# Kernel optimization log

Measured on AMD Instinct MI355X. Metric: run time of the kernel, lower is better.

## Reference

```python
import jax, jax.numpy as jnp
import numpy as np

B, N_P, N_S, D, H = 8, 512, 512, 512, 8
HD = D // H
SCALE = HD ** -0.5


def setup_inputs() -> dict:
    key = jax.random.key(0)
    ks = jax.random.split(key, 16)
    init = lambda k, shape, fan_in: jax.random.normal(k, shape, jnp.float32) * (1.0 / np.sqrt(fan_in))
    return {
        "piece_embeds": jax.random.normal(ks[0], (B, N_P, D), jnp.float32),
        "slot_embeds": jax.random.normal(ks[1], (B, N_S, D), jnp.float32),
        "mask": jax.random.randint(ks[2], (B, N_P, N_S), 0, 2, jnp.int32),
        "spatial_bias": jax.random.normal(ks[3], (B, N_P, N_S), jnp.float32),
        "Wq": init(ks[4], (D, D), D), "bq": jnp.zeros((D,), jnp.float32),
        "Wk": init(ks[5], (D, D), D), "bk": jnp.zeros((D,), jnp.float32),
        "Wv": init(ks[6], (D, D), D), "bv": jnp.zeros((D,), jnp.float32),
        "Wo": init(ks[7], (D, D), D), "bo": jnp.zeros((D,), jnp.float32),
        "Wc": init(ks[8], (2 * D,), 2 * D), "bc": jnp.zeros((), jnp.float32),
        "Wval": init(ks[9], (D,), D), "bval": jnp.zeros((), jnp.float32),
    }


def reference(piece_embeds, slot_embeds, mask, spatial_bias,
              Wq, bq, Wk, bk, Wv, bv, Wo, bo, Wc, bc, Wval, bval):
    Bv, Np, Dv = piece_embeds.shape
    Ns = slot_embeds.shape[1]
    Q = (piece_embeds @ Wq + bq).reshape(Bv, Np, H, HD)
    K = (slot_embeds @ Wk + bk).reshape(Bv, Ns, H, HD)
    V = (slot_embeds @ Wv + bv).reshape(Bv, Ns, H, HD)
    # per-head scores, scaled, then averaged over heads (non-standard)
    scores = jnp.einsum('bphd,bshd->bps', Q, K) * (SCALE / H)
    scores = scores + spatial_bias
    scores = jnp.where(mask == 0, jnp.float32(-1e9), scores)
    attn_probs = jax.nn.softmax(scores, axis=-1)  # dropout is identity at eval
    # the original expand*mul*sum over [B,Np,Ns,H,HD] == this contraction
    attn_output = jnp.einsum('bps,bshd->bphd', attn_probs, V).reshape(Bv, Np, Dv)
    output = attn_output @ Wo + bo
    value = (output.mean(axis=1) @ Wval + bval)[:, None]  # [B,1]
    # concat-linear over pairs == split-weight GEMMs with broadcast add
    Wc_p, Wc_s = Wc[:Dv], Wc[Dv:]
    compatibility = (piece_embeds @ Wc_p)[:, :, None] + (slot_embeds @ Wc_s)[:, None, :] + bc
    return scores, value, compatibility
```

## Files before the change

### kernel.cpp

```cpp
#include <hip/hip_runtime.h>
#include <math.h>

#define NP 512
#define NS 512
#define DD 512
#define INV64 0.015625f
#define NEGBIG -1000000000.0f
#define LOG2E 1.4426950408889634f

#define WS_SLOTBF 0
#define WS_WQBF   1048576
#define WS_WKBF   1179648
#define WS_MTBF   1310720
#define WS_WV     1441792
#define WS_U      1442304
#define WS_WQBK   1442816
#define WS_WKBQ   1443328
#define WS_VV     1443840
#define WS_A      1447936
#define WS_E      1452032
#define WS_CP     1456128
#define WS_CS     1460224
#define WS_Z      1464320
#define WS_W      1468416
#define WS_SC     1472512

#define OUT_SCORES 0
#define OUT_VALUE  2097152
#define OUT_COMP   2097160

typedef short bf16x8 __attribute__((ext_vector_type(8)));
typedef float f32x4 __attribute__((ext_vector_type(4)));

__device__ __forceinline__ short f2bf(float f) {
  unsigned u = __builtin_bit_cast(unsigned, f);
  u += 0x7fffu + ((u >> 16) & 1u);
  return (short)(u >> 16);
}

__device__ __forceinline__ void async_copy16(const void* g, void* l) {
  __builtin_amdgcn_global_load_lds(
      (const __attribute__((address_space(1))) unsigned int*)g,
      (__attribute__((address_space(3))) unsigned int*)l, 16, 0, 0);
}

__device__ __forceinline__ float dot8(float4 a0, float4 a1, float4 b0, float4 b1) {
  return a0.x * b0.x + a0.y * b0.y + a0.z * b0.z + a0.w * b0.w +
         a1.x * b1.x + a1.y * b1.y + a1.z * b1.z + a1.w * b1.w;
}

__device__ __forceinline__ float wave_red(float s) {
#pragma unroll
  for (int o = 32; o; o >>= 1) s += __shfl_xor(s, o);
  return s;
}

__device__ inline float wave_dot512(const float* __restrict__ x,
                                    const float* __restrict__ y, int lane) {
  float4 x0 = *(const float4*)&x[lane * 8];
  float4 x1 = *(const float4*)&x[lane * 8 + 4];
  float4 y0 = *(const float4*)&y[lane * 8];
  float4 y1 = *(const float4*)&y[lane * 8 + 4];
  return wave_red(dot8(x0, x1, y0, y1));
}

__global__ __launch_bounds__(256) void kA(
    const float* __restrict__ Wo, const float* __restrict__ Wval,
    const float* __restrict__ Wq, const float* __restrict__ bk,
    const float* __restrict__ Wk, const float* __restrict__ bq,
    const float* __restrict__ bo, const float* __restrict__ bval,
    float* __restrict__ ws, short* __restrict__ wqb, short* __restrict__ wkb) {
  int blk = blockIdx.x;
  if (blk < 385) {
    int wid = blk * 4 + (threadIdx.x >> 6);
    int lane = threadIdx.x & 63;
    if (wid >= 1538) return;
    const float *x, *y;
    float* dst;
    float extra = 0.f;
    int r = wid & 511;
    if (wid < 512)       { x = Wo + (size_t)r * DD; y = Wval; dst = ws + WS_WV + r; }
    else if (wid < 1024) { x = Wq + (size_t)r * DD; y = bk;   dst = ws + WS_WQBK + r; }
    else if (wid < 1536) { x = Wk + (size_t)r * DD; y = bq;   dst = ws + WS_WKBQ + r; }
    else if (wid == 1536){ x = bo; y = Wval; dst = ws + WS_SC + 1; extra = *bval; }
    else                 { x = bq; y = bk;   dst = ws + WS_SC + 2; }
    float s = wave_dot512(x, y, lane);
    if (lane == 0) *dst = s + extra;
  } else {
    int t = (blk - 385) * 256 + threadIdx.x;
    const float* src;
    short* dst;
    int off;
    if (t < 32768) { src = Wq; dst = wqb; off = t * 8; }
    else           { src = Wk; dst = wkb; off = (t - 32768) * 8; }
    float4 v0 = *(const float4*)&src[off];
    float4 v1 = *(const float4*)&src[off + 4];
    bf16x8 o;
    o[0] = f2bf(v0.x); o[1] = f2bf(v0.y); o[2] = f2bf(v0.z); o[3] = f2bf(v0.w);
    o[4] = f2bf(v1.x); o[5] = f2bf(v1.y); o[6] = f2bf(v1.z); o[7] = f2bf(v1.w);
    *(bf16x8*)&dst[off] = o;
  }
}

template <int NG>
__device__ __forceinline__ void stage_tile4(const short* __restrict__ G,
                                            short* lds, int r0, int k0, int wave,
                                            int lane) {
#pragma unroll
  for (int h = 0; h < NG / 256; ++h) {
    int s = h * 256 + wave * 64 + lane;
    int row = s >> 2;
    int g = (s & 3) ^ ((row >> 1) & 3);
    async_copy16(G + (size_t)(r0 + row) * DD + k0 + g * 8,
                 lds + (size_t)(h * 256 + wave * 64) * 8);
  }
}

__global__ __launch_bounds__(256) void kB(
    const float* __restrict__ Wv, const float* __restrict__ bv,
    const short* __restrict__ wkb, const short* __restrict__ wqb,
    float* __restrict__ ws, short* __restrict__ mtb) {
  __shared__ short As[2][128 * 32];
  __shared__ short Bs[2][64 * 32];
  if (blockIdx.x < 129) {
    int wid = blockIdx.x * 4 + (threadIdx.x >> 6);
    if (wid >= 513) return;
    int lane = threadIdx.x & 63;
    const float* wv = ws + WS_WV;
    const float *x, *y;
    float* dst;
    if (wid < 512) { x = Wv + (size_t)wid * DD; y = wv; dst = ws + WS_U + wid; }
    else           { x = bv; y = wv; dst = ws + WS_SC + 0; }
    float s = wave_dot512(x, y, lane);
    if (lane == 0) *dst = s;
    return;
  }
  int gb = blockIdx.x - 129;
  const int m0 = (gb & 3) * 128, n0 = (gb >> 2) * 64;
  const int wave = threadIdx.x >> 6, lane = threadIdx.x & 63;
  const int wr = wave >> 1, wc = wave & 1;
  const int li = lane & 15, g = lane >> 4;
  f32x4 acc[4][2] = {};
  stage_tile4<512>(wkb, &As[0][0], m0, 0, wave, lane);
  stage_tile4<256>(wqb, &Bs[0][0], n0, 0, wave, lane);
  __syncthreads();
  int buf = 0;
  for (int k0 = 0; k0 < DD; k0 += 32) {
    if (k0 + 32 < DD) {
      stage_tile4<512>(wkb, &As[buf ^ 1][0], m0, k0 + 32, wave, lane);
      stage_tile4<256>(wqb, &Bs[buf ^ 1][0], n0, k0 + 32, wave, lane);
    }
    bf16x8 af[4], bfr[2];
#pragma unroll
    for (int am = 0; am < 4; ++am) {
      int row = wr * 64 + am * 16 + li;
      int gp = g ^ ((row >> 1) & 3);
      af[am] = *(const bf16x8*)&As[buf][row * 32 + gp * 8];
    }
#pragma unroll
    for (int bn = 0; bn < 2; ++bn) {
      int row = wc * 32 + bn * 16 + li;
      int gp = g ^ ((row >> 1) & 3);
      bfr[bn] = *(const bf16x8*)&Bs[buf][row * 32 + gp * 8];
    }
#pragma unroll
    for (int am = 0; am < 4; ++am)
#pragma unroll
      for (int bn = 0; bn < 2; ++bn)
        acc[am][bn] = __builtin_amdgcn_mfma_f32_16x16x32_bf16(
            af[am], bfr[bn], acc[am][bn], 0, 0, 0);
    __syncthreads();
    buf ^= 1;
  }
#pragma unroll
  for (int am = 0; am < 4; ++am)
#pragma unroll
    for (int i = 0; i < 4; ++i) {
      int grow = m0 + wr * 64 + am * 16 + g * 4 + i;
#pragma unroll
      for (int bn = 0; bn < 2; ++bn) {
        int gcol = n0 + wc * 32 + bn * 16 + li;
        mtb[(size_t)grow * DD + gcol] = f2bf(acc[am][bn][i]);
      }
    }
}

__global__ __launch_bounds__(256) void kC(
    const float* __restrict__ piece, const float* __restrict__ slot,
    const float* __restrict__ Wc, float* __restrict__ ws,
    short* __restrict__ pbf, short* __restrict__ sbf) {
  int lane = threadIdx.x & 63;
  if (blockIdx.x < 1024) {
    int wid = blockIdx.x * 4 + (threadIdx.x >> 6);
    const float* row = piece + (size_t)wid * DD;
    float4 x0 = *(const float4*)&row[lane * 8];
    float4 x1 = *(const float4*)&row[lane * 8 + 4];
    bf16x8 o;
    o[0] = f2bf(x0.x); o[1] = f2bf(x0.y); o[2] = f2bf(x0.z); o[3] = f2bf(x0.w);
    o[4] = f2bf(x1.x); o[5] = f2bf(x1.y); o[6] = f2bf(x1.z); o[7] = f2bf(x1.w);
    *(bf16x8*)&pbf[(size_t)wid * DD + lane * 8] = o;
    const float* y = ws + WS_WQBK;
    float4 y0 = *(const float4*)&y[lane * 8];
    float4 y1 = *(const float4*)&y[lane * 8 + 4];
    float4 c0 = *(const float4*)&Wc[lane * 8];
    float4 c1 = *(const float4*)&Wc[lane * 8 + 4];
    float da = wave_red(dot8(x0, x1, y0, y1));
    float dc = wave_red(dot8(x0, x1, c0, c1));
    if (lane == 0) { ws[WS_A + wid] = da; ws[WS_CP + wid] = dc; }
  } else if (blockIdx.x < 2048) {
    int wid = (blockIdx.x - 1024) * 4 + (threadIdx.x >> 6);
    const float* row = slot + (size_t)wid * DD;
    float4 x0 = *(const float4*)&row[lane * 8];
    float4 x1 = *(const float4*)&row[lane * 8 + 4];
    bf16x8 o;
    o[0] = f2bf(x0.x); o[1] = f2bf(x0.y); o[2] = f2bf(x0.z); o[3] = f2bf(x0.w);
    o[4] = f2bf(x1.x); o[5] = f2bf(x1.y); o[6] = f2bf(x1.z); o[7] = f2bf(x1.w);
    *(bf16x8*)&sbf[(size_t)wid * DD + lane * 8] = o;
    const float* y = ws + WS_WKBQ;
    float4 y0 = *(const float4*)&y[lane * 8];
    float4 y1 = *(const float4*)&y[lane * 8 + 4];
    const float* u = ws + WS_U;
    float4 u0 = *(const float4*)&u[lane * 8];
    float4 u1 = *(const float4*)&u[lane * 8 + 4];
    const float* c = Wc + DD;
    float4 c0 = *(const float4*)&c[lane * 8];
    float4 c1 = *(const float4*)&c[lane * 8 + 4];
    float de = wave_red(dot8(x0, x1, y0, y1));
    float dv = wave_red(dot8(x0, x1, u0, u1));
    float dc = wave_red(dot8(x0, x1, c0, c1));
    if (lane == 0) {
      ws[WS_E + wid] = de;
      ws[WS_VV + wid] = dv + ws[WS_SC + 0];
      ws[WS_CS + wid] = dc;
    }
  } else {
    float4 zz = make_float4(0.f, 0.f, 0.f, 0.f);
#pragma unroll
    for (int k = 0; k < 8; ++k)
      *(float4*)&ws[WS_Z + (threadIdx.x * 8 + k) * 4] = zz;
  }
}

template <int MODE>
__global__ __launch_bounds__(512) void k_gemm8(
    const short* __restrict__ A, const short* __restrict__ B,
    short* __restrict__ Cb, const float* __restrict__ ws_,
    const float* __restrict__ sbias, const int* __restrict__ maskp,
    float* __restrict__ out, float* __restrict__ zarr,
    float* __restrict__ warr) {
  __shared__ short As[2][128 * 64];
  __shared__ short Bs[2][64 * 64];
  const int wave = threadIdx.x >> 6, lane = threadIdx.x & 63;
  const int wr = wave >> 1, wc = wave & 1;
  const int li = lane & 15, g = lane >> 4;
  const int id = blockIdx.x;
  int b, m0, n0;
  if (MODE == 0) { b = 0; m0 = (id & 31) * 128; n0 = (id >> 5) * 64; }
  else           { b = id & 7; m0 = ((id >> 3) & 3) * 128; n0 = (id >> 5) * 64; }
  const short* Ab = A + (size_t)b * NP * DD;
  const short* Bb = B + (size_t)b * NS * DD;
  f32x4 acc[2][2] = {};

  auto stage = [&](int bufi, int k0) {
#pragma unroll
    for (int h = 0; h < 2; ++h) {
      int s = h * 512 + wave * 64 + lane;
      int row = s >> 3;
      int gsrc = (s & 7) ^ (row & 7);
      async_copy16(Ab + (size_t)(m0 + row) * DD + k0 + gsrc * 8,
                   &As[bufi][(h * 512 + wave * 64) * 8]);
    }
    {
      int s = wave * 64 + lane;
      int row = s >> 3;
      int gsrc = (s & 7) ^ (row & 7);
      async_copy16(Bb + (size_t)(n0 + row) * DD + k0 + gsrc * 8,
                   &Bs[bufi][(wave * 64) * 8]);
    }
  };

  stage(0, 0);
  __syncthreads();
  int buf = 0;
  for (int k0 = 0; k0 < DD; k0 += 64) {
    if (k0 + 64 < DD) stage(buf ^ 1, k0 + 64);
    bf16x8 af[2][2], bfv[2][2];
#pragma unroll
    for (int kk = 0; kk < 2; ++kk) {
#pragma unroll
      for (int am = 0; am < 2; ++am) {
        int row = wr * 32 + am * 16 + li;
        int slot = row * 8 + ((kk * 4 + g) ^ (row & 7));
        af[am][kk] = *(const bf16x8*)&As[buf][slot * 8];
      }
#pragma unroll
      for (int bn = 0; bn < 2; ++bn) {
        int row = wc * 32 + bn * 16 + li;
        int slot = row * 8 + ((kk * 4 + g) ^ (row & 7));
        bfv[bn][kk] = *(const bf16x8*)&Bs[buf][slot * 8];
      }
    }
#pragma unroll
    for (int kk = 0; kk < 2; ++kk)
#pragma unroll
      for (int am = 0; am < 2; ++am)
#pragma unroll
        for (int bn = 0; bn < 2; ++bn)
          acc[am][bn] = __builtin_amdgcn_mfma_f32_16x16x32_bf16(
              af[am][kk], bfv[bn][kk], acc[am][bn], 0, 0, 0);
    __syncthreads();
    buf ^= 1;
  }

  if (MODE == 0) {
#pragma unroll
    for (int am = 0; am < 2; ++am)
#pragma unroll
      for (int i = 0; i < 4; ++i) {
        int grow = m0 + wr * 32 + am * 16 + g * 4 + i;
#pragma unroll
        for (int bn = 0; bn < 2; ++bn) {
          int gcol = n0 + wc * 32 + bn * 16 + li;
          Cb[(size_t)grow * DD + gcol] = f2bf(acc[am][bn][i]);
        }
      }
  } else {
    const float sbb = ws_[WS_SC + 2];
    const float* evp = ws_ + WS_E + b * NS;
    const float* vvp = ws_ + WS_VV + b * NS;
    const float* avp = ws_ + WS_A + b * NP;
    float ev[2], vvl[2];
#pragma unroll
    for (int bn = 0; bn < 2; ++bn) {
      int scol = n0 + wc * 32 + bn * 16 + li;
      ev[bn] = evp[scol];
      vvl[bn] = vvp[scol];
    }
#pragma unroll
    for (int am = 0; am < 2; ++am)
#pragma unroll
      for (int i = 0; i < 4; ++i) {
        int p = m0 + wr * 32 + am * 16 + g * 4 + i;
        float av = avp[p] + sbb;
        float zp = 0.f, wp = 0.f;
#pragma unroll
        for (int bn = 0; bn < 2; ++bn) {
          int scol = n0 + wc * 32 + bn * 16 + li;
          size_t idx = ((size_t)b * NP + p) * NS + scol;
          float v = fmaf(acc[am][bn][i] + av + ev[bn], INV64, sbias[idx]);
          v = (maskp[idx] == 0) ? NEGBIG : v;
          out[OUT_SCORES + idx] = v;
          float e = exp2f(v * LOG2E);
          zp += e;
          wp += e * vvl[bn];
        }
#pragma unroll
        for (int o = 1; o < 16; o <<= 1) {
          zp += __shfl_xor(zp, o);
          wp += __shfl_xor(wp, o);
        }
        if (li == 0) {
          atomicAdd(&zarr[b * NP + p], zp);
          atomicAdd(&warr[b * NP + p], wp);
        }
      }
  }
}

__global__ __launch_bounds__(256) void kG(const float* __restrict__ ws,
                                          const float* __restrict__ bc,
                                          float* __restrict__ out) {
  if (blockIdx.x < 2048) {
    int idx = blockIdx.x * 256 + threadIdx.x;
    int lin = idx << 2;
    int s = lin & (NS - 1);
    int p = (lin >> 9) & (NP - 1);
    int bb = lin >> 18;
    float cp = ws[WS_CP + bb * NP + p];
    float4 cs = *(const float4*)&ws[WS_CS + bb * NS + s];
    float bcv = *bc;
    float4 o = make_float4(cp + cs.x + bcv, cp + cs.y + bcv, cp + cs.z + bcv,
                           cp + cs.w + bcv);
    *(float4*)&out[OUT_COMP + lin] = o;
  } else {
    int tid = threadIdx.x;
    int bb = tid >> 5, j = tid & 31;
    const float* zp = ws + WS_Z + bb * NP;
    const float* wp = ws + WS_W + bb * NP;
    float s = 0.f;
#pragma unroll
    for (int k = 0; k < 16; ++k) {
      int p = k * 32 + j;
      s += wp[p] / zp[p];
    }
#pragma unroll
    for (int o = 16; o; o >>= 1) s += __shfl_xor(s, o);
    if (j == 0) out[OUT_VALUE + bb] = s * (1.0f / NP) + ws[WS_SC + 1];
  }
}

extern "C" void kernel_launch(void* const* d_in, const int* in_sizes, int n_in,
                              void* d_out, int out_size, void* d_ws,
                              size_t ws_size, hipStream_t stream) {
  const float* piece = (const float*)d_in[0];
  const float* slot = (const float*)d_in[1];
  const int* mask = (const int*)d_in[2];
  const float* sbias = (const float*)d_in[3];
  const float* Wq = (const float*)d_in[4];
  const float* bq = (const float*)d_in[5];
  const float* Wk = (const float*)d_in[6];
  const float* bk = (const float*)d_in[7];
  const float* Wv = (const float*)d_in[8];
  const float* bv = (const float*)d_in[9];
  const float* Wo = (const float*)d_in[10];
  const float* bo = (const float*)d_in[11];
  const float* Wc = (const float*)d_in[12];
  const float* bc = (const float*)d_in[13];
  const float* Wval = (const float*)d_in[14];
  const float* bval = (const float*)d_in[15];
  float* out = (float*)d_out;
  float* ws = (float*)d_ws;

  short* pbf = (short*)out;
  short* tbf = (short*)(out + OUT_COMP);
  short* sbf = (short*)(ws + WS_SLOTBF);
  short* wqb = (short*)(ws + WS_WQBF);
  short* wkb = (short*)(ws + WS_WKBF);
  short* mtb = (short*)(ws + WS_MTBF);

  hipLaunchKernelGGL(kA, dim3(641), dim3(256), 0, stream,
                     Wo, Wval, Wq, bk, Wk, bq, bo, bval, ws, wqb, wkb);
  hipLaunchKernelGGL(kB, dim3(161), dim3(256), 0, stream, Wv, bv, wkb, wqb, ws, mtb);
  hipLaunchKernelGGL(kC, dim3(2049), dim3(256), 0, stream, piece, slot, Wc, ws, pbf, sbf);
  hipLaunchKernelGGL((k_gemm8<0>), dim3(256), dim3(512), 0, stream,
                     pbf, mtb, tbf, (const float*)nullptr, (const float*)nullptr,
                     (const int*)nullptr, (float*)nullptr, (float*)nullptr,
                     (float*)nullptr);
  hipLaunchKernelGGL((k_gemm8<1>), dim3(256), dim3(512), 0, stream,
                     tbf, sbf, (short*)nullptr, ws, sbias, mask, out,
                     ws + WS_Z, ws + WS_W);
  hipLaunchKernelGGL(kG, dim3(2049), dim3(256), 0, stream, ws, bc, out);
}
```

Before: 52.86 us.

## Fuse bf16 conversions and row dots into GEMM staging, merge compatibility and value epilogues

The fp32-to-bf16 conversion kernels for Wq/Wk, piece and slot embeddings are removed. Each GEMM now loads fp32 tiles directly, converts them in registers while staging into padded LDS, and computes the per-row dot products (A, CP, E, VV, CS) from the same loaded values. The compatibility broadcast write is moved into the score GEMM epilogue, and the final value reduction runs in the last block through an atomic counter. This cuts the launch count from six to four and removes several full-tensor passes through memory. The cost is synchronous fp32 loads in the staging path, which lose the async LDS copies, plus extra register pressure.

```diff
diff --git a/kernel.cpp b/kernel.cpp
--- a/kernel.cpp
+++ b/kernel.cpp
@@ -8,22 +8,18 @@
 #define NEGBIG -1000000000.0f
 #define LOG2E 1.4426950408889634f
 
-#define WS_SLOTBF 0
-#define WS_WQBF   1048576
-#define WS_WKBF   1179648
-#define WS_MTBF   1310720
-#define WS_WV     1441792
-#define WS_U      1442304
-#define WS_WQBK   1442816
-#define WS_WKBQ   1443328
-#define WS_VV     1443840
-#define WS_A      1447936
-#define WS_E      1452032
-#define WS_CP     1456128
-#define WS_CS     1460224
-#define WS_Z      1464320
-#define WS_W      1468416
-#define WS_SC     1472512
+#define WS_MTBF   0
+#define WS_TBF    131072
+#define WS_WV     1179648
+#define WS_U      1180160
+#define WS_WQBK   1180672
+#define WS_WKBQ   1181184
+#define WS_A      1181696
+#define WS_CP     1185792
+#define WS_Z      1189888
+#define WS_W      1193984
+#define WS_SC     1198080
+#define WS_CNT    1198084
 
 #define OUT_SCORES 0
 #define OUT_VALUE  2097152
@@ -36,6 +32,13 @@
   unsigned u = __builtin_bit_cast(unsigned, f);
   u += 0x7fffu + ((u >> 16) & 1u);
   return (short)(u >> 16);
+}
+
+__device__ __forceinline__ bf16x8 cvt8(float4 a, float4 b) {
+  bf16x8 o;
+  o[0] = f2bf(a.x); o[1] = f2bf(a.y); o[2] = f2bf(a.z); o[3] = f2bf(a.w);
+  o[4] = f2bf(b.x); o[5] = f2bf(b.y); o[6] = f2bf(b.z); o[7] = f2bf(b.w);
+  return o;
 }
 
 __device__ __forceinline__ void async_copy16(const void* g, void* l) {
@@ -69,214 +72,66 @@
     const float* __restrict__ Wq, const float* __restrict__ bk,
     const float* __restrict__ Wk, const float* __restrict__ bq,
     const float* __restrict__ bo, const float* __restrict__ bval,
-    float* __restrict__ ws, short* __restrict__ wqb, short* __restrict__ wkb) {
-  int blk = blockIdx.x;
-  if (blk < 385) {
-    int wid = blk * 4 + (threadIdx.x >> 6);
-    int lane = threadIdx.x & 63;
-    if (wid >= 1538) return;
-    const float *x, *y;
-    float* dst;
-    float extra = 0.f;
-    int r = wid & 511;
-    if (wid < 512)       { x = Wo + (size_t)r * DD; y = Wval; dst = ws + WS_WV + r; }
-    else if (wid < 1024) { x = Wq + (size_t)r * DD; y = bk;   dst = ws + WS_WQBK + r; }
-    else if (wid < 1536) { x = Wk + (size_t)r * DD; y = bq;   dst = ws + WS_WKBQ + r; }
-    else if (wid == 1536){ x = bo; y = Wval; dst = ws + WS_SC + 1; extra = *bval; }
-    else                 { x = bq; y = bk;   dst = ws + WS_SC + 2; }
-    float s = wave_dot512(x, y, lane);
-    if (lane == 0) *dst = s + extra;
-  } else {
-    int t = (blk - 385) * 256 + threadIdx.x;
-    const float* src;
-    short* dst;
-    int off;
-    if (t < 32768) { src = Wq; dst = wqb; off = t * 8; }
-    else           { src = Wk; dst = wkb; off = (t - 32768) * 8; }
-    float4 v0 = *(const float4*)&src[off];
-    float4 v1 = *(const float4*)&src[off + 4];
-    bf16x8 o;
-    o[0] = f2bf(v0.x); o[1] = f2bf(v0.y); o[2] = f2bf(v0.z); o[3] = f2bf(v0.w);
-    o[4] = f2bf(v1.x); o[5] = f2bf(v1.y); o[6] = f2bf(v1.z); o[7] = f2bf(v1.w);
-    *(bf16x8*)&dst[off] = o;
-  }
-}
-
-template <int NG>
-__device__ __forceinline__ void stage_tile4(const short* __restrict__ G,
-                                            short* lds, int r0, int k0, int wave,
-                                            int lane) {
-#pragma unroll
-  for (int h = 0; h < NG / 256; ++h) {
-    int s = h * 256 + wave * 64 + lane;
-    int row = s >> 2;
-    int g = (s & 3) ^ ((row >> 1) & 3);
-    async_copy16(G + (size_t)(r0 + row) * DD + k0 + g * 8,
-                 lds + (size_t)(h * 256 + wave * 64) * 8);
-  }
-}
-
-__global__ __launch_bounds__(256) void kB(
+    float* __restrict__ ws) {
+  int wid = blockIdx.x * 4 + (threadIdx.x >> 6);
+  int lane = threadIdx.x & 63;
+  if (wid >= 1538) return;
+  const float *x, *y;
+  float* dst;
+  float extra = 0.f;
+  int r = wid & 511;
+  if (wid < 512)        { x = Wo + (size_t)r * DD; y = Wval; dst = ws + WS_WV + r; }
+  else if (wid < 1024)  { x = Wq + (size_t)r * DD; y = bk;   dst = ws + WS_WQBK + r; }
+  else if (wid < 1536)  { x = Wk + (size_t)r * DD; y = bq;   dst = ws + WS_WKBQ + r; }
+  else if (wid == 1536) { x = bo; y = Wval; dst = ws + WS_SC + 1; extra = *bval; }
+  else                  { x = bq; y = bk;   dst = ws + WS_SC + 2; }
+  float s = wave_dot512(x, y, lane);
+  if (lane == 0) *dst = s + extra;
+}
+
+__global__ __launch_bounds__(512) void kB(
+    const float* __restrict__ Wk, const float* __restrict__ Wq,
     const float* __restrict__ Wv, const float* __restrict__ bv,
-    const short* __restrict__ wkb, const short* __restrict__ wqb,
     float* __restrict__ ws, short* __restrict__ mtb) {
-  __shared__ short As[2][128 * 32];
-  __shared__ short Bs[2][64 * 32];
-  if (blockIdx.x < 129) {
-    int wid = blockIdx.x * 4 + (threadIdx.x >> 6);
-    if (wid >= 513) return;
-    int lane = threadIdx.x & 63;
-    const float* wv = ws + WS_WV;
-    const float *x, *y;
-    float* dst;
-    if (wid < 512) { x = Wv + (size_t)wid * DD; y = wv; dst = ws + WS_U + wid; }
-    else           { x = bv; y = wv; dst = ws + WS_SC + 0; }
-    float s = wave_dot512(x, y, lane);
-    if (lane == 0) *dst = s;
+  __shared__ alignas(16) short As[2][128 * 72];
+  __shared__ alignas(16) short Bs[2][64 * 72];
+  const int blk = blockIdx.x;
+  const int wave = threadIdx.x >> 6, lane = threadIdx.x & 63;
+  if (blk >= 32) {
+    if (blk < 97) {
+      int wid = (blk - 32) * 8 + wave;
+      if (wid < 512) {
+        float s = wave_dot512(Wv + (size_t)wid * DD, ws + WS_WV, lane);
+        if (lane == 0) ws[WS_U + wid] = s;
+      } else if (wid == 512) {
+        float s = wave_dot512(bv, ws + WS_WV, lane);
+        if (lane == 0) ws[WS_SC + 0] = s;
+      }
+    } else {
+      int t = (blk - 97) * 512 + threadIdx.x;
+      float4 zz = make_float4(0.f, 0.f, 0.f, 0.f);
+      *(float4*)&ws[WS_Z + t * 4] = zz;
+      *(float4*)&ws[WS_W + t * 4] = zz;
+      if (blk == 97 && threadIdx.x == 0) *(unsigned*)(ws + WS_CNT) = 0u;
+    }
     return;
   }
-  int gb = blockIdx.x - 129;
-  const int m0 = (gb & 3) * 128, n0 = (gb >> 2) * 64;
-  const int wave = threadIdx.x >> 6, lane = threadIdx.x & 63;
   const int wr = wave >> 1, wc = wave & 1;
   const int li = lane & 15, g = lane >> 4;
-  f32x4 acc[4][2] = {};
-  stage_tile4<512>(wkb, &As[0][0], m0, 0, wave, lane);
-  stage_tile4<256>(wqb, &Bs[0][0], n0, 0, wave, lane);
-  __syncthreads();
-  int buf = 0;
-  for (int k0 = 0; k0 < DD; k0 += 32) {
-    if (k0 + 32 < DD) {
-      stage_tile4<512>(wkb, &As[buf ^ 1][0], m0, k0 + 32, wave, lane);
-      stage_tile4<256>(wqb, &Bs[buf ^ 1][0], n0, k0 + 32, wave, lane);
-    }
-    bf16x8 af[4], bfr[2];
-#pragma unroll
-    for (int am = 0; am < 4; ++am) {
-      int row = wr * 64 + am * 16 + li;
-      int gp = g ^ ((row >> 1) & 3);
-      af[am] = *(const bf16x8*)&As[buf][row * 32 + gp * 8];
-    }
-#pragma unroll
-    for (int bn = 0; bn < 2; ++bn) {
-      int row = wc * 32 + bn * 16 + li;
-      int gp = g ^ ((row >> 1) & 3);
-      bfr[bn] = *(const bf16x8*)&Bs[buf][row * 32 + gp * 8];
-    }
-#pragma unroll
-    for (int am = 0; am < 4; ++am)
-#pragma unroll
-      for (int bn = 0; bn < 2; ++bn)
-        acc[am][bn] = __builtin_amdgcn_mfma_f32_16x16x32_bf16(
-            af[am], bfr[bn], acc[am][bn], 0, 0, 0);
-    __syncthreads();
-    buf ^= 1;
-  }
-#pragma unroll
-  for (int am = 0; am < 4; ++am)
-#pragma unroll
-    for (int i = 0; i < 4; ++i) {
-      int grow = m0 + wr * 64 + am * 16 + g * 4 + i;
-#pragma unroll
-      for (int bn = 0; bn < 2; ++bn) {
-        int gcol = n0 + wc * 32 + bn * 16 + li;
-        mtb[(size_t)grow * DD + gcol] = f2bf(acc[am][bn][i]);
-      }
-    }
-}
-
-__global__ __launch_bounds__(256) void kC(
-    const float* __restrict__ piece, const float* __restrict__ slot,
-    const float* __restrict__ Wc, float* __restrict__ ws,
-    short* __restrict__ pbf, short* __restrict__ sbf) {
-  int lane = threadIdx.x & 63;
-  if (blockIdx.x < 1024) {
-    int wid = blockIdx.x * 4 + (threadIdx.x >> 6);
-    const float* row = piece + (size_t)wid * DD;
-    float4 x0 = *(const float4*)&row[lane * 8];
-    float4 x1 = *(const float4*)&row[lane * 8 + 4];
-    bf16x8 o;
-    o[0] = f2bf(x0.x); o[1] = f2bf(x0.y); o[2] = f2bf(x0.z); o[3] = f2bf(x0.w);
-    o[4] = f2bf(x1.x); o[5] = f2bf(x1.y); o[6] = f2bf(x1.z); o[7] = f2bf(x1.w);
-    *(bf16x8*)&pbf[(size_t)wid * DD + lane * 8] = o;
-    const float* y = ws + WS_WQBK;
-    float4 y0 = *(const float4*)&y[lane * 8];
-    float4 y1 = *(const float4*)&y[lane * 8 + 4];
-    float4 c0 = *(const float4*)&Wc[lane * 8];
-    float4 c1 = *(const float4*)&Wc[lane * 8 + 4];
-    float da = wave_red(dot8(x0, x1, y0, y1));
-    float dc = wave_red(dot8(x0, x1, c0, c1));
-    if (lane == 0) { ws[WS_A + wid] = da; ws[WS_CP + wid] = dc; }
-  } else if (blockIdx.x < 2048) {
-    int wid = (blockIdx.x - 1024) * 4 + (threadIdx.x >> 6);
-    const float* row = slot + (size_t)wid * DD;
-    float4 x0 = *(const float4*)&row[lane * 8];
-    float4 x1 = *(const float4*)&row[lane * 8 + 4];
-    bf16x8 o;
-    o[0] = f2bf(x0.x); o[1] = f2bf(x0.y); o[2] = f2bf(x0.z); o[3] = f2bf(x0.w);
-    o[4] = f2bf(x1.x); o[5] = f2bf(x1.y); o[6] = f2bf(x1.z); o[7] = f2bf(x1.w);
-    *(bf16x8*)&sbf[(size_t)wid * DD + lane * 8] = o;
-    const float* y = ws + WS_WKBQ;
-    float4 y0 = *(const float4*)&y[lane * 8];
-    float4 y1 = *(const float4*)&y[lane * 8 + 4];
-    const float* u = ws + WS_U;
-    float4 u0 = *(const float4*)&u[lane * 8];
-    float4 u1 = *(const float4*)&u[lane * 8 + 4];
-    const float* c = Wc + DD;
-    float4 c0 = *(const float4*)&c[lane * 8];
-    float4 c1 = *(const float4*)&c[lane * 8 + 4];
-    float de = wave_red(dot8(x0, x1, y0, y1));
-    float dv = wave_red(dot8(x0, x1, u0, u1));
-    float dc = wave_red(dot8(x0, x1, c0, c1));
-    if (lane == 0) {
-      ws[WS_E + wid] = de;
-      ws[WS_VV + wid] = dv + ws[WS_SC + 0];
-      ws[WS_CS + wid] = dc;
-    }
-  } else {
-    float4 zz = make_float4(0.f, 0.f, 0.f, 0.f);
-#pragma unroll
-    for (int k = 0; k < 8; ++k)
-      *(float4*)&ws[WS_Z + (threadIdx.x * 8 + k) * 4] = zz;
-  }
-}
-
-template <int MODE>
-__global__ __launch_bounds__(512) void k_gemm8(
-    const short* __restrict__ A, const short* __restrict__ B,
-    short* __restrict__ Cb, const float* __restrict__ ws_,
-    const float* __restrict__ sbias, const int* __restrict__ maskp,
-    float* __restrict__ out, float* __restrict__ zarr,
-    float* __restrict__ warr) {
-  __shared__ short As[2][128 * 64];
-  __shared__ short Bs[2][64 * 64];
-  const int wave = threadIdx.x >> 6, lane = threadIdx.x & 63;
-  const int wr = wave >> 1, wc = wave & 1;
-  const int li = lane & 15, g = lane >> 4;
-  const int id = blockIdx.x;
-  int b, m0, n0;
-  if (MODE == 0) { b = 0; m0 = (id & 31) * 128; n0 = (id >> 5) * 64; }
-  else           { b = id & 7; m0 = ((id >> 3) & 3) * 128; n0 = (id >> 5) * 64; }
-  const short* Ab = A + (size_t)b * NP * DD;
-  const short* Bb = B + (size_t)b * NS * DD;
+  const int m0 = (blk & 3) * 128, n0 = (blk >> 2) * 64;
+  const int arow = threadIdx.x >> 2, aseg = threadIdx.x & 3;
+  const int brow = threadIdx.x >> 3, bseg = threadIdx.x & 7;
   f32x4 acc[2][2] = {};
 
   auto stage = [&](int bufi, int k0) {
-#pragma unroll
-    for (int h = 0; h < 2; ++h) {
-      int s = h * 512 + wave * 64 + lane;
-      int row = s >> 3;
-      int gsrc = (s & 7) ^ (row & 7);
-      async_copy16(Ab + (size_t)(m0 + row) * DD + k0 + gsrc * 8,
-                   &As[bufi][(h * 512 + wave * 64) * 8]);
-    }
-    {
-      int s = wave * 64 + lane;
-      int row = s >> 3;
-      int gsrc = (s & 7) ^ (row & 7);
-      async_copy16(Bb + (size_t)(n0 + row) * DD + k0 + gsrc * 8,
-                   &Bs[bufi][(wave * 64) * 8]);
-    }
+    const float* sa = Wk + (size_t)(m0 + arow) * DD + k0 + aseg * 16;
+    float4 a0 = *(const float4*)sa, a1 = *(const float4*)(sa + 4);
+    float4 a2 = *(const float4*)(sa + 8), a3 = *(const float4*)(sa + 12);
+    *(bf16x8*)&As[bufi][arow * 72 + aseg * 16] = cvt8(a0, a1);
+    *(bf16x8*)&As[bufi][arow * 72 + aseg * 16 + 8] = cvt8(a2, a3);
+    const float* sb = Wq + (size_t)(n0 + brow) * DD + k0 + bseg * 8;
+    float4 b0 = *(const float4*)sb, b1 = *(const float4*)(sb + 4);
+    *(bf16x8*)&Bs[bufi][brow * 72 + bseg * 8] = cvt8(b0, b1);
   };
 
   stage(0, 0);
@@ -288,17 +143,11 @@
 #pragma unroll
     for (int kk = 0; kk < 2; ++kk) {
 #pragma unroll
-      for (int am = 0; am < 2; ++am) {
-        int row = wr * 32 + am * 16 + li;
-        int slot = row * 8 + ((kk * 4 + g) ^ (row & 7));
-        af[am][kk] = *(const bf16x8*)&As[buf][slot * 8];
-      }
-#pragma unroll
-      for (int bn = 0; bn < 2; ++bn) {
-        int row = wc * 32 + bn * 16 + li;
-        int slot = row * 8 + ((kk * 4 + g) ^ (row & 7));
-        bfv[bn][kk] = *(const bf16x8*)&Bs[buf][slot * 8];
-      }
+      for (int am = 0; am < 2; ++am)
+        af[am][kk] = *(const bf16x8*)&As[buf][(wr * 32 + am * 16 + li) * 72 + kk * 32 + g * 8];
+#pragma unroll
+      for (int bn = 0; bn < 2; ++bn)
+        bfv[bn][kk] = *(const bf16x8*)&Bs[buf][(wc * 32 + bn * 16 + li) * 72 + kk * 32 + g * 8];
     }
 #pragma unroll
     for (int kk = 0; kk < 2; ++kk)
@@ -311,91 +160,231 @@
     __syncthreads();
     buf ^= 1;
   }
-
-  if (MODE == 0) {
-#pragma unroll
-    for (int am = 0; am < 2; ++am)
-#pragma unroll
-      for (int i = 0; i < 4; ++i) {
-        int grow = m0 + wr * 32 + am * 16 + g * 4 + i;
-#pragma unroll
-        for (int bn = 0; bn < 2; ++bn) {
-          int gcol = n0 + wc * 32 + bn * 16 + li;
-          Cb[(size_t)grow * DD + gcol] = f2bf(acc[am][bn][i]);
-        }
-      }
-  } else {
-    const float sbb = ws_[WS_SC + 2];
-    const float* evp = ws_ + WS_E + b * NS;
-    const float* vvp = ws_ + WS_VV + b * NS;
-    const float* avp = ws_ + WS_A + b * NP;
-    float ev[2], vvl[2];
-#pragma unroll
-    for (int bn = 0; bn < 2; ++bn) {
-      int scol = n0 + wc * 32 + bn * 16 + li;
-      ev[bn] = evp[scol];
-      vvl[bn] = vvp[scol];
-    }
-#pragma unroll
-    for (int am = 0; am < 2; ++am)
-#pragma unroll
-      for (int i = 0; i < 4; ++i) {
-        int p = m0 + wr * 32 + am * 16 + g * 4 + i;
-        float av = avp[p] + sbb;
-        float zp = 0.f, wp = 0.f;
-#pragma unroll
-        for (int bn = 0; bn < 2; ++bn) {
-          int scol = n0 + wc * 32 + bn * 16 + li;
-          size_t idx = ((size_t)b * NP + p) * NS + scol;
-          float v = fmaf(acc[am][bn][i] + av + ev[bn], INV64, sbias[idx]);
-          v = (maskp[idx] == 0) ? NEGBIG : v;
-          out[OUT_SCORES + idx] = v;
-          float e = exp2f(v * LOG2E);
-          zp += e;
-          wp += e * vvl[bn];
-        }
-#pragma unroll
-        for (int o = 1; o < 16; o <<= 1) {
-          zp += __shfl_xor(zp, o);
-          wp += __shfl_xor(wp, o);
-        }
-        if (li == 0) {
-          atomicAdd(&zarr[b * NP + p], zp);
-          atomicAdd(&warr[b * NP + p], wp);
-        }
-      }
-  }
-}
-
-__global__ __launch_bounds__(256) void kG(const float* __restrict__ ws,
-                                          const float* __restrict__ bc,
-                                          float* __restrict__ out) {
-  if (blockIdx.x < 2048) {
-    int idx = blockIdx.x * 256 + threadIdx.x;
-    int lin = idx << 2;
-    int s = lin & (NS - 1);
-    int p = (lin >> 9) & (NP - 1);
-    int bb = lin >> 18;
-    float cp = ws[WS_CP + bb * NP + p];
-    float4 cs = *(const float4*)&ws[WS_CS + bb * NS + s];
-    float bcv = *bc;
-    float4 o = make_float4(cp + cs.x + bcv, cp + cs.y + bcv, cp + cs.z + bcv,
-                           cp + cs.w + bcv);
-    *(float4*)&out[OUT_COMP + lin] = o;
-  } else {
-    int tid = threadIdx.x;
-    int bb = tid >> 5, j = tid & 31;
-    const float* zp = ws + WS_Z + bb * NP;
-    const float* wp = ws + WS_W + bb * NP;
+#pragma unroll
+  for (int am = 0; am < 2; ++am)
+#pragma unroll
+    for (int i = 0; i < 4; ++i) {
+      int grow = m0 + wr * 32 + am * 16 + g * 4 + i;
+#pragma unroll
+      for (int bn = 0; bn < 2; ++bn) {
+        int gcol = n0 + wc * 32 + bn * 16 + li;
+        mtb[(size_t)grow * DD + gcol] = f2bf(acc[am][bn][i]);
+      }
+    }
+}
+
+__global__ __launch_bounds__(512) void kT(
+    const float* __restrict__ piece, const short* __restrict__ mtb,
+    const float* __restrict__ Wc, float* __restrict__ ws,
+    short* __restrict__ tbf) {
+  __shared__ alignas(16) short As[2][128 * 72];
+  __shared__ alignas(16) short Bs[2][64 * 64];
+  const int id = blockIdx.x;
+  const int m0 = (id & 31) * 128, n0 = (id >> 5) * 64;
+  const int wave = threadIdx.x >> 6, lane = threadIdx.x & 63;
+  const int wr = wave >> 1, wc = wave & 1;
+  const int li = lane & 15, g = lane >> 4;
+  const int arow = threadIdx.x >> 2, aseg = threadIdx.x & 3;
+  const bool do_dots = (n0 == 0);
+  float a_acc = 0.f, cp_acc = 0.f;
+  f32x4 acc[2][2] = {};
+
+  auto stage = [&](int bufi, int k0) {
+    const float* sa = piece + (size_t)(m0 + arow) * DD + k0 + aseg * 16;
+    float4 a0 = *(const float4*)sa, a1 = *(const float4*)(sa + 4);
+    float4 a2 = *(const float4*)(sa + 8), a3 = *(const float4*)(sa + 12);
+    *(bf16x8*)&As[bufi][arow * 72 + aseg * 16] = cvt8(a0, a1);
+    *(bf16x8*)&As[bufi][arow * 72 + aseg * 16 + 8] = cvt8(a2, a3);
+    if (do_dots) {
+      const float* yq = ws + WS_WQBK + k0 + aseg * 16;
+      const float* yc = Wc + k0 + aseg * 16;
+      a_acc += dot8(a0, a1, *(const float4*)yq, *(const float4*)(yq + 4)) +
+               dot8(a2, a3, *(const float4*)(yq + 8), *(const float4*)(yq + 12));
+      cp_acc += dot8(a0, a1, *(const float4*)yc, *(const float4*)(yc + 4)) +
+                dot8(a2, a3, *(const float4*)(yc + 8), *(const float4*)(yc + 12));
+    }
+    int s = wave * 64 + lane;
+    int row = s >> 3;
+    int gsrc = (s & 7) ^ (row & 7);
+    async_copy16(mtb + (size_t)(n0 + row) * DD + k0 + gsrc * 8,
+                 &Bs[bufi][(wave * 64) * 8]);
+  };
+
+  stage(0, 0);
+  __syncthreads();
+  int buf = 0;
+  for (int k0 = 0; k0 < DD; k0 += 64) {
+    if (k0 + 64 < DD) stage(buf ^ 1, k0 + 64);
+    bf16x8 af[2][2], bfv[2][2];
+#pragma unroll
+    for (int kk = 0; kk < 2; ++kk) {
+#pragma unroll
+      for (int am = 0; am < 2; ++am)
+        af[am][kk] = *(const bf16x8*)&As[buf][(wr * 32 + am * 16 + li) * 72 + kk * 32 + g * 8];
+#pragma unroll
+      for (int bn = 0; bn < 2; ++bn) {
+        int row = wc * 32 + bn * 16 + li;
+        bfv[bn][kk] = *(const bf16x8*)&Bs[buf][(row * 8 + ((kk * 4 + g) ^ (row & 7))) * 8];
+      }
+    }
+#pragma unroll
+    for (int kk = 0; kk < 2; ++kk)
+#pragma unroll
+      for (int am = 0; am < 2; ++am)
+#pragma unroll
+        for (int bn = 0; bn < 2; ++bn)
+          acc[am][bn] = __builtin_amdgcn_mfma_f32_16x16x32_bf16(
+              af[am][kk], bfv[bn][kk], acc[am][bn], 0, 0, 0);
+    __syncthreads();
+    buf ^= 1;
+  }
+  if (do_dots) {
+    a_acc += __shfl_xor(a_acc, 1);  a_acc += __shfl_xor(a_acc, 2);
+    cp_acc += __shfl_xor(cp_acc, 1); cp_acc += __shfl_xor(cp_acc, 2);
+    if (aseg == 0) {
+      ws[WS_A + m0 + arow] = a_acc;
+      ws[WS_CP + m0 + arow] = cp_acc;
+    }
+  }
+#pragma unroll
+  for (int am = 0; am < 2; ++am)
+#pragma unroll
+    for (int i = 0; i < 4; ++i) {
+      int grow = m0 + wr * 32 + am * 16 + g * 4 + i;
+#pragma unroll
+      for (int bn = 0; bn < 2; ++bn) {
+        int gcol = n0 + wc * 32 + bn * 16 + li;
+        tbf[(size_t)grow * DD + gcol] = f2bf(acc[am][bn][i]);
+      }
+    }
+}
+
+__global__ __launch_bounds__(512) void kS(
+    const short* __restrict__ tbf, const float* __restrict__ slotp,
+    const float* __restrict__ sbias, const int* __restrict__ maskp,
+    const float* __restrict__ Wc, const float* __restrict__ bc,
+    float* __restrict__ ws, float* __restrict__ out) {
+  __shared__ alignas(16) short As[2][128 * 64];
+  __shared__ alignas(16) short Bs[2][64 * 72];
+  __shared__ float e_l[64], vv_l[64], cs_l[64];
+  __shared__ unsigned lastflag;
+  const int id = blockIdx.x;
+  const int b = id & 7, m0 = ((id >> 3) & 3) * 128, n0 = (id >> 5) * 64;
+  const int wave = threadIdx.x >> 6, lane = threadIdx.x & 63;
+  const int wr = wave >> 1, wc = wave & 1;
+  const int li = lane & 15, g = lane >> 4;
+  const int brow = threadIdx.x >> 3, bseg = threadIdx.x & 7;
+  float e_acc = 0.f, vv_acc = 0.f, cs_acc = 0.f;
+  f32x4 acc[2][2] = {};
+
+  auto stage = [&](int bufi, int k0) {
+#pragma unroll
+    for (int h = 0; h < 2; ++h) {
+      int s = h * 512 + wave * 64 + lane;
+      int row = s >> 3;
+      int gsrc = (s & 7) ^ (row & 7);
+      async_copy16(tbf + (size_t)(b * NP + m0 + row) * DD + k0 + gsrc * 8,
+                   &As[bufi][(h * 512 + wave * 64) * 8]);
+    }
+    const float* sb = slotp + (size_t)(b * NS + n0 + brow) * DD + k0 + bseg * 8;
+    float4 b0 = *(const float4*)sb, b1 = *(const float4*)(sb + 4);
+    *(bf16x8*)&Bs[bufi][brow * 72 + bseg * 8] = cvt8(b0, b1);
+    const float* yk = ws + WS_WKBQ + k0 + bseg * 8;
+    const float* yu = ws + WS_U + k0 + bseg * 8;
+    const float* yc = Wc + DD + k0 + bseg * 8;
+    e_acc += dot8(b0, b1, *(const float4*)yk, *(const float4*)(yk + 4));
+    vv_acc += dot8(b0, b1, *(const float4*)yu, *(const float4*)(yu + 4));
+    cs_acc += dot8(b0, b1, *(const float4*)yc, *(const float4*)(yc + 4));
+  };
+
+  stage(0, 0);
+  __syncthreads();
+  int buf = 0;
+  for (int k0 = 0; k0 < DD; k0 += 64) {
+    if (k0 + 64 < DD) stage(buf ^ 1, k0 + 64);
+    bf16x8 af[2][2], bfv[2][2];
+#pragma unroll
+    for (int kk = 0; kk < 2; ++kk) {
+#pragma unroll
+      for (int am = 0; am < 2; ++am) {
+        int row = wr * 32 + am * 16 + li;
+        af[am][kk] = *(const bf16x8*)&As[buf][(row * 8 + ((kk * 4 + g) ^ (row & 7))) * 8];
+      }
+#pragma unroll
+      for (int bn = 0; bn < 2; ++bn)
+        bfv[bn][kk] = *(const bf16x8*)&Bs[buf][(wc * 32 + bn * 16 + li) * 72 + kk * 32 + g * 8];
+    }
+#pragma unroll
+    for (int kk = 0; kk < 2; ++kk)
+#pragma unroll
+      for (int am = 0; am < 2; ++am)
+#pragma unroll
+        for (int bn = 0; bn < 2; ++bn)
+          acc[am][bn] = __builtin_amdgcn_mfma_f32_16x16x32_bf16(
+              af[am][kk], bfv[bn][kk], acc[am][bn], 0, 0, 0);
+    __syncthreads();
+    buf ^= 1;
+  }
+
+  e_acc += __shfl_xor(e_acc, 1); e_acc += __shfl_xor(e_acc, 2); e_acc += __shfl_xor(e_acc, 4);
+  vv_acc += __shfl_xor(vv_acc, 1); vv_acc += __shfl_xor(vv_acc, 2); vv_acc += __shfl_xor(vv_acc, 4);
+  cs_acc += __shfl_xor(cs_acc, 1); cs_acc += __shfl_xor(cs_acc, 2); cs_acc += __shfl_xor(cs_acc, 4);
+  if (bseg == 0) {
+    e_l[brow] = e_acc;
+    vv_l[brow] = vv_acc + ws[WS_SC + 0];
+    cs_l[brow] = cs_acc;
+  }
+  __syncthreads();
+
+  const float sbb = ws[WS_SC + 2];
+  const float bcv = *bc;
+#pragma unroll
+  for (int am = 0; am < 2; ++am)
+#pragma unroll
+    for (int i = 0; i < 4; ++i) {
+      int p = m0 + wr * 32 + am * 16 + g * 4 + i;
+      float av = ws[WS_A + b * NP + p] + sbb;
+      float cpv = ws[WS_CP + b * NP + p] + bcv;
+      float zp = 0.f, wp = 0.f;
+#pragma unroll
+      for (int bn = 0; bn < 2; ++bn) {
+        int lcol = wc * 32 + bn * 16 + li;
+        size_t idx = ((size_t)b * NP + p) * NS + n0 + lcol;
+        float v = fmaf(acc[am][bn][i] + av + e_l[lcol], INV64, sbias[idx]);
+        v = (maskp[idx] == 0) ? NEGBIG : v;
+        out[OUT_SCORES + idx] = v;
+        float ee = exp2f(v * LOG2E);
+        zp += ee;
+        wp += ee * vv_l[lcol];
+        out[OUT_COMP + idx] = cpv + cs_l[lcol];
+      }
+#pragma unroll
+      for (int o = 1; o < 16; o <<= 1) {
+        zp += __shfl_xor(zp, o);
+        wp += __shfl_xor(wp, o);
+      }
+      if (li == 0) {
+        atomicAdd(&ws[WS_Z + b * NP + p], zp);
+        atomicAdd(&ws[WS_W + b * NP + p], wp);
+      }
+    }
+
+  __threadfence();
+  if (threadIdx.x == 0) lastflag = atomicAdd((unsigned*)(ws + WS_CNT), 1u);
+  __syncthreads();
+  if (lastflag == 255) {
+    int vb = threadIdx.x >> 6, l = threadIdx.x & 63;
     float s = 0.f;
 #pragma unroll
-    for (int k = 0; k < 16; ++k) {
-      int p = k * 32 + j;
-      s += wp[p] / zp[p];
-    }
-#pragma unroll
-    for (int o = 16; o; o >>= 1) s += __shfl_xor(s, o);
-    if (j == 0) out[OUT_VALUE + bb] = s * (1.0f / NP) + ws[WS_SC + 1];
+    for (int j = 0; j < 8; ++j) {
+      int p = l + j * 64;
+      float zz = atomicAdd(&ws[WS_Z + vb * NP + p], 0.f);
+      float ww = atomicAdd(&ws[WS_W + vb * NP + p], 0.f);
+      s += ww / zz;
+    }
+#pragma unroll
+    for (int o = 32; o; o >>= 1) s += __shfl_xor(s, o);
+    if (l == 0) out[OUT_VALUE + vb] = s * (1.0f / NP) + ws[WS_SC + 1];
   }
 }
 
@@ -421,23 +410,13 @@
   float* out = (float*)d_out;
   float* ws = (float*)d_ws;
 
-  short* pbf = (short*)out;
-  short* tbf = (short*)(out + OUT_COMP);
-  short* sbf = (short*)(ws + WS_SLOTBF);
-  short* wqb = (short*)(ws + WS_WQBF);
-  short* wkb = (short*)(ws + WS_WKBF);
   short* mtb = (short*)(ws + WS_MTBF);
-
-  hipLaunchKernelGGL(kA, dim3(641), dim3(256), 0, stream,
-                     Wo, Wval, Wq, bk, Wk, bq, bo, bval, ws, wqb, wkb);
-  hipLaunchKernelGGL(kB, dim3(161), dim3(256), 0, stream, Wv, bv, wkb, wqb, ws, mtb);
-  hipLaunchKernelGGL(kC, dim3(2049), dim3(256), 0, stream, piece, slot, Wc, ws, pbf, sbf);
-  hipLaunchKernelGGL((k_gemm8<0>), dim3(256), dim3(512), 0, stream,
-                     pbf, mtb, tbf, (const float*)nullptr, (const float*)nullptr,
-                     (const int*)nullptr, (float*)nullptr, (float*)nullptr,
-                     (float*)nullptr);
-  hipLaunchKernelGGL((k_gemm8<1>), dim3(256), dim3(512), 0, stream,
-                     tbf, sbf, (short*)nullptr, ws, sbias, mask, out,
-                     ws + WS_Z, ws + WS_W);
-  hipLaunchKernelGGL(kG, dim3(2049), dim3(256), 0, stream, ws, bc, out);
-}
+  short* tbf = (short*)(ws + WS_TBF);
+
+  hipLaunchKernelGGL(kA, dim3(385), dim3(256), 0, stream,
+                     Wo, Wval, Wq, bk, Wk, bq, bo, bval, ws);
+  hipLaunchKernelGGL(kB, dim3(99), dim3(512), 0, stream, Wk, Wq, Wv, bv, ws, mtb);
+  hipLaunchKernelGGL(kT, dim3(256), dim3(512), 0, stream, piece, mtb, Wc, ws, tbf);
+  hipLaunchKernelGGL(kS, dim3(256), dim3(512), 0, stream, tbf, slot, sbias, mask,
+                     Wc, bc, ws, out);
+}
```

Result: slower. 106.5 us (+101.4%).
